# Performance work log

Measured on AMD Instinct MI355X. Metric: run time of the kernel, lower is better.

## Reference

```python
import jax, jax.numpy as jnp
import numpy as np

N, B, C, H = 1024, 4, 256, 8
D = C // H


def _make_boxes(k):
    u = jax.random.uniform(k, (N, 4), dtype=jnp.float32)
    x1 = u[:, 0] * 500.0
    y1 = u[:, 1] * 500.0
    x2 = x1 + u[:, 2] * 200.0 + 1.0
    y2 = y1 + u[:, 3] * 200.0 + 1.0
    return jnp.stack([x1, y1, x2, y2], axis=1)


def setup_inputs() -> dict:
    rng = jax.random.key(0)
    ks = jax.random.split(rng, 10)
    s = 1.0 / np.sqrt(C)
    return {
        "query": jax.random.normal(ks[0], (N, B, C), dtype=jnp.float32),
        "key": jax.random.normal(ks[1], (N, B, C), dtype=jnp.float32),
        "value": jax.random.normal(ks[2], (N, B, C), dtype=jnp.float32),
        "q_boxes": _make_boxes(ks[3]),
        "k_boxes": _make_boxes(ks[4]),
        "Wq": jax.random.normal(ks[5], (C, C), dtype=jnp.float32) * s,
        "Wk": jax.random.normal(ks[6], (C, C), dtype=jnp.float32) * s,
        "Wv": jax.random.normal(ks[7], (C, C), dtype=jnp.float32) * s,
        "pos_w": jax.random.normal(ks[8], (H, 64), dtype=jnp.float32) * 0.125,
        "pos_b": jax.random.normal(ks[9], (H,), dtype=jnp.float32) * 0.01,
    }


def _position_bias(qb, kb, pos_w, pos_b):
    # extract_position_matrix: boxes are x1y1x2y2, shapes [N,4]
    cx, cy = 0.5 * (qb[:, 0] + qb[:, 2]), 0.5 * (qb[:, 1] + qb[:, 3])
    w, h = qb[:, 2] - qb[:, 0] + 1.0, qb[:, 3] - qb[:, 1] + 1.0
    cxr, cyr = 0.5 * (kb[:, 0] + kb[:, 2]), 0.5 * (kb[:, 1] + kb[:, 3])
    wr, hr = kb[:, 2] - kb[:, 0] + 1.0, kb[:, 3] - kb[:, 1] + 1.0
    dx = jnp.log(jnp.abs((cx[:, None] - cxr[None, :]) / w[:, None]) + 1e-3)
    dy = jnp.log(jnp.abs((cy[:, None] - cyr[None, :]) / h[:, None]) + 1e-3)
    dw = jnp.log(w[:, None] / wr[None, :])
    dh = jnp.log(h[:, None] / hr[None, :])
    pm = jnp.stack([dx, dy, dw, dh], axis=2)  # [N, N, 4]
    # extract_position_embedding: feat_dim=64 -> 8 sinusoid frequencies
    dim_mat = 1000.0 ** (jnp.arange(8, dtype=jnp.float32) * (8.0 / 64.0))
    div = pm[..., None] * 100.0 / dim_mat  # [N, N, 4, 8]
    emb = jnp.concatenate([jnp.sin(div), jnp.cos(div)], axis=3)
    emb = emb.reshape(pm.shape[0], pm.shape[1], 64)  # [N, N, 64]
    # 1x1 Conv2d(64 -> H) over the [64, N, N] map == channel matmul
    pe = jnp.einsum('nmc,hc->hnm', emb, pos_w) + pos_b[:, None, None]
    return jnp.log(jax.nn.relu(pe) + 1e-6)  # [H, N, N]


def reference(query, key, value, q_boxes, k_boxes, Wq, Wk, Wv, pos_w, pos_b):
    n, b, c = query.shape
    d = c // H

    def proj(x, W):
        # nn.Linear (no bias): x @ W.T ; reshape (N,B,H,D) -> (B,H,N,D)
        return (x @ W.T).reshape(n, b, H, d).transpose(1, 2, 0, 3)

    q = proj(query, Wq)
    k = proj(key, Wk)
    v = proj(value, Wv)
    # cosine normalization of q and k
    q = q / jnp.linalg.norm(q, axis=-1, keepdims=True)
    k = k / jnp.linalg.norm(k, axis=-1, keepdims=True)
    attn_reg = jax.nn.softmax(jnp.einsum('bhnd,bhmd->bhnm', q, k), axis=-1)
    # log of relu'd conv position embedding added AFTER softmax (as in source)
    attn = attn_reg + _position_bias(q_boxes, k_boxes, pos_w, pos_b)[None]
    out = jnp.einsum('bhnm,bhmd->bhnd', attn, v)  # [B,H,N,D]
    out = out.transpose(0, 2, 1, 3).reshape(b, n, c).transpose(1, 0, 2)  # [N,B,C]
    return (out, attn)
```

## Files before the change

kernel.cpp:

```cpp
#include <hip/hip_runtime.h>
#include <hip/hip_bf16.h>
#include <math.h>

#define PN 1024
#define PB 4
#define PC 256
#define PH 8
#define PD 32

typedef __attribute__((ext_vector_type(8))) short bf16x8;
typedef __attribute__((ext_vector_type(4))) float f32x4;

__device__ __forceinline__ unsigned short f2b(float f) {
    unsigned int u = __builtin_bit_cast(unsigned int, f);
    unsigned int r = (u + 0x7fffu + ((u >> 16) & 1u)) >> 16;
    return (unsigned short)r;
}
__device__ __forceinline__ float b2f(unsigned short u) {
    return __builtin_bit_cast(float, ((unsigned int)u) << 16);
}

__global__ __launch_bounds__(256) void cvt_kernel(
    const float* __restrict__ q, const float* __restrict__ k, const float* __restrict__ v,
    const float* __restrict__ wq, const float* __restrict__ wk, const float* __restrict__ wv,
    unsigned short* __restrict__ xq, unsigned short* __restrict__ xk, unsigned short* __restrict__ xv,
    unsigned short* __restrict__ wqb, unsigned short* __restrict__ wkb, unsigned short* __restrict__ wvb)
{
    int g = blockIdx.x * 256 + threadIdx.x;
    const float* src; unsigned short* dst; int off;
    if (g < 262144)      { src = q; dst = xq; off = g; }
    else if (g < 524288) { src = k; dst = xk; off = g - 262144; }
    else if (g < 786432) { src = v; dst = xv; off = g - 524288; }
    else {
        int r = g - 786432; int t = r >> 14; off = r & 16383;
        src = (t == 0) ? wq : (t == 1) ? wk : wv;
        dst = (t == 0) ? wqb : (t == 1) ? wkb : wvb;
    }
    float4 f = ((const float4*)src)[off];
    ushort4 o; o.x = f2b(f.x); o.y = f2b(f.y); o.z = f2b(f.z); o.w = f2b(f.w);
    ((ushort4*)dst)[off] = o;
}

__global__ __launch_bounds__(256) void proj_mfma(
    const unsigned short* __restrict__ xq, const unsigned short* __restrict__ xk, const unsigned short* __restrict__ xv,
    const unsigned short* __restrict__ wq, const unsigned short* __restrict__ wk, const unsigned short* __restrict__ wv,
    unsigned short* __restrict__ qb, unsigned short* __restrict__ kb, unsigned short* __restrict__ vt)
{
    const int z = blockIdx.z;
    const unsigned short* X = (z == 0) ? xq : (z == 1) ? xk : xv;
    const unsigned short* W = (z == 0) ? wq : (z == 1) ? wk : wv;

    const int row0 = blockIdx.x * 64, col0 = blockIdx.y * 64;
    const int tid = threadIdx.x;
    const int w = tid >> 6, l = tid & 63;
    const int l15 = l & 15, lg = l >> 4;
    const int wm = w >> 1, wn = w & 1;

    f32x4 acc[2][2];
    #pragma unroll
    for (int a = 0; a < 2; a++)
        #pragma unroll
        for (int b = 0; b < 2; b++) acc[a][b] = (f32x4){0.f, 0.f, 0.f, 0.f};

    #pragma unroll
    for (int ks = 0; ks < 8; ks++) {
        int koff = ks * 32 + lg * 8;
        bf16x8 a0 = *(const bf16x8*)(X + (size_t)(row0 + wm * 32 + l15) * 256 + koff);
        bf16x8 a1 = *(const bf16x8*)(X + (size_t)(row0 + wm * 32 + 16 + l15) * 256 + koff);
        bf16x8 b0 = *(const bf16x8*)(W + (size_t)(col0 + wn * 32 + l15) * 256 + koff);
        bf16x8 b1 = *(const bf16x8*)(W + (size_t)(col0 + wn * 32 + 16 + l15) * 256 + koff);
        acc[0][0] = __builtin_amdgcn_mfma_f32_16x16x32_bf16(a0, b0, acc[0][0], 0, 0, 0);
        acc[0][1] = __builtin_amdgcn_mfma_f32_16x16x32_bf16(a0, b1, acc[0][1], 0, 0, 0);
        acc[1][0] = __builtin_amdgcn_mfma_f32_16x16x32_bf16(a1, b0, acc[1][0], 0, 0, 0);
        acc[1][1] = __builtin_amdgcn_mfma_f32_16x16x32_bf16(a1, b1, acc[1][1], 0, 0, 0);
    }

    #pragma unroll
    for (int as = 0; as < 2; as++) {
        #pragma unroll
        for (int bs = 0; bs < 2; bs++) {
            #pragma unroll
            for (int r = 0; r < 4; r++) {
                int Xrow = row0 + wm * 32 + as * 16 + lg * 4 + r;
                int c = col0 + wn * 32 + bs * 16 + l15;
                int n = Xrow >> 2, bb = Xrow & 3, hh = c >> 5, dd = c & 31;
                unsigned short val = f2b(acc[as][bs][r]);
                if (z == 0)      qb[((size_t)((bb * 8 + hh) * 1024 + n)) * 32 + dd] = val;
                else if (z == 1) kb[((size_t)((bb * 8 + hh) * 1024 + n)) * 32 + dd] = val;
                else             vt[((size_t)((bb * 8 + hh) * 32 + dd)) * 1024 + n] = val;
            }
        }
    }
}

__global__ __launch_bounds__(256) void norm_kernel(unsigned short* __restrict__ qb,
                                                   unsigned short* __restrict__ kb)
{
    int idx = blockIdx.x * 256 + threadIdx.x;
    unsigned short* p = (idx < 32768) ? qb + (size_t)idx * 32
                                      : kb + (size_t)(idx - 32768) * 32;
    const unsigned int* pu = (const unsigned int*)p;
    float g[32]; float s2 = 0.f;
    #pragma unroll
    for (int j = 0; j < 16; j++) {
        unsigned int u = pu[j];
        g[2 * j]     = b2f((unsigned short)(u & 0xffff));
        g[2 * j + 1] = b2f((unsigned short)(u >> 16));
        s2 += g[2 * j] * g[2 * j] + g[2 * j + 1] * g[2 * j + 1];
    }
    float inv = rsqrtf(s2);
    unsigned int* po = (unsigned int*)p;
    #pragma unroll
    for (int j = 0; j < 16; j++) {
        unsigned int lo = f2b(g[2 * j] * inv);
        unsigned int hi = f2b(g[2 * j + 1] * inv);
        po[j] = lo | (hi << 16);
    }
}

__global__ __launch_bounds__(256) void bias_kernel(
    const float* __restrict__ qbx, const float* __restrict__ kbx,
    const float* __restrict__ pw, const float* __restrict__ pb,
    unsigned short* __restrict__ biasb)
{
    __shared__ float4 pwS[128];
    __shared__ float pbS[8];
    int tid = threadIdx.x;
    if (tid < 128) pwS[tid] = ((const float4*)pw)[tid];
    if (tid < 8) pbS[tid] = pb[tid];
    __syncthreads();

    int idx = blockIdx.x * 256 + tid;
    int n = idx >> 10, m = idx & 1023;

    float4 qx = ((const float4*)qbx)[n];
    float4 kx = ((const float4*)kbx)[m];

    float cx = 0.5f * (qx.x + qx.z), cy = 0.5f * (qx.y + qx.w);
    float w  = qx.z - qx.x + 1.0f,   hh = qx.w - qx.y + 1.0f;
    float cxr = 0.5f * (kx.x + kx.z), cyr = 0.5f * (kx.y + kx.w);
    float wr  = kx.z - kx.x + 1.0f,   hr  = kx.w - kx.y + 1.0f;

    float pm[4];
    pm[0] = __logf(fabsf((cx - cxr) / w) + 1e-3f);
    pm[1] = __logf(fabsf((cy - cyr) / hh) + 1e-3f);
    pm[2] = __logf(w / wr);
    pm[3] = __logf(hh / hr);

    const float inv[8] = {100.f, 42.1696503f, 17.7827941f, 7.49894209f,
                          3.16227766f, 1.33352143f, 0.562341325f, 0.237137371f};

    float emb[64];
    #pragma unroll
    for (int p = 0; p < 4; p++) {
        #pragma unroll
        for (int i = 0; i < 8; i++) {
            float a = pm[p] * inv[i];
            emb[p * 16 + i]     = __sinf(a);
            emb[p * 16 + 8 + i] = __cosf(a);
        }
    }

    #pragma unroll
    for (int h = 0; h < PH; h++) {
        float acc = pbS[h];
        #pragma unroll
        for (int c4 = 0; c4 < 16; c4++) {
            float4 w4 = pwS[h * 16 + c4];
            acc += emb[c4 * 4 + 0] * w4.x + emb[c4 * 4 + 1] * w4.y
                 + emb[c4 * 4 + 2] * w4.z + emb[c4 * 4 + 3] * w4.w;
        }
        float bv = __logf(fmaxf(acc, 0.f) + 1e-6f);
        biasb[((size_t)(h * 1024 + n)) * 1024 + m] = f2b(bv);
    }
}

#define SBS 1032

__global__ __launch_bounds__(512, 4) void attn_kernel(
    const unsigned short* __restrict__ qb, const unsigned short* __restrict__ kb,
    const unsigned short* __restrict__ vt, const unsigned short* __restrict__ biasb,
    float* __restrict__ out, float* __restrict__ attn_out)
{
    __shared__ unsigned short Sb[32][SBS];
    __shared__ float part[8][16][17];

    const int bh = blockIdx.y;
    const int b = bh >> 3, h = bh & 7;
    const int n0 = blockIdx.x * 32;
    const int tid = threadIdx.x;
    const int w = tid >> 6, l = tid & 63;
    const int l15 = l & 15, lg = l >> 4;

    {
        const int wq = w >> 2, wk = w & 3;
        const int qrow = n0 + wq * 16 + l15;
        bf16x8 aq = *(const bf16x8*)(qb + ((size_t)(bh << 10) + qrow) * 32 + lg * 8);
        #pragma unroll 4
        for (int t = 0; t < 16; ++t) {
            int key = wk * 256 + t * 16 + l15;
            bf16x8 bk = *(const bf16x8*)(kb + ((size_t)(bh << 10) + key) * 32 + lg * 8);
            f32x4 acc = (f32x4){0.f, 0.f, 0.f, 0.f};
            acc = __builtin_amdgcn_mfma_f32_16x16x32_bf16(aq, bk, acc, 0, 0, 0);
            int colb = wk * 256 + t * 16 + l15;
            #pragma unroll
            for (int r = 0; r < 4; ++r)
                Sb[wq * 16 + lg * 4 + r][colb] = f2b(acc[r]);
        }
    }
    __syncthreads();

    {
        for (int rr = 0; rr < 4; ++rr) {
            int r = w * 4 + rr;
            float s[16];
            #pragma unroll
            for (int i = 0; i < 16; ++i) s[i] = b2f(Sb[r][l + 64 * i]);
            float mx = s[0];
            #pragma unroll
            for (int i = 1; i < 16; ++i) mx = fmaxf(mx, s[i]);
            #pragma unroll
            for (int off = 32; off > 0; off >>= 1) mx = fmaxf(mx, __shfl_xor(mx, off));
            float e[16], sum = 0.f;
            #pragma unroll
            for (int i = 0; i < 16; ++i) { e[i] = __expf(s[i] - mx); sum += e[i]; }
            #pragma unroll
            for (int off = 32; off > 0; off >>= 1) sum += __shfl_xor(sum, off);
            float invs = 1.f / sum;

            const unsigned short* brow = biasb + ((size_t)(h * 1024 + n0 + r)) * 1024;
            float* arow = attn_out + ((size_t)(bh * 1024 + n0 + r)) * 1024;
            #pragma unroll
            for (int i = 0; i < 16; ++i) {
                int m = l + 64 * i;
                float a = e[i] * invs + b2f(brow[m]);
                arow[m] = a;
                Sb[r][m] = f2b(a);
            }
        }
    }
    __syncthreads();

    {
        const int tile = w >> 1, kh = w & 1;
        const int qs = tile >> 1, ds = tile & 1;
        f32x4 acc = (f32x4){0.f, 0.f, 0.f, 0.f};
        const unsigned short* vrow = vt + ((size_t)(bh * 32 + ds * 16 + l15) << 10);
        const unsigned short* srow = &Sb[qs * 16 + l15][0];
        #pragma unroll 4
        for (int st = 0; st < 16; ++st) {
            int m0 = kh * 512 + st * 32 + lg * 8;
            bf16x8 ap = *(const bf16x8*)(srow + m0);
            bf16x8 bv = *(const bf16x8*)(vrow + m0);
            acc = __builtin_amdgcn_mfma_f32_16x16x32_bf16(ap, bv, acc, 0, 0, 0);
        }
        #pragma unroll
        for (int r = 0; r < 4; ++r) part[w][lg * 4 + r][l15] = acc[r];
    }
    __syncthreads();

    {
        #pragma unroll
        for (int e = 0; e < 2; ++e) {
            int idx = tid + e * 512;
            int q = idx >> 5, d = idx & 31;
            int w0 = ((q >> 4) * 2 + (d >> 4)) << 1;
            float v = part[w0][q & 15][d & 15] + part[w0 + 1][q & 15][d & 15];
            out[((size_t)(n0 + q) * PB + b) * PC + h * PD + d] = v;
        }
    }
}

extern "C" void kernel_launch(void* const* d_in, const int* in_sizes, int n_in,
                              void* d_out, int out_size, void* d_ws, size_t ws_size,
                              hipStream_t stream)
{
    const float* query   = (const float*)d_in[0];
    const float* key     = (const float*)d_in[1];
    const float* value   = (const float*)d_in[2];
    const float* q_boxes = (const float*)d_in[3];
    const float* k_boxes = (const float*)d_in[4];
    const float* Wq      = (const float*)d_in[5];
    const float* Wk      = (const float*)d_in[6];
    const float* Wv      = (const float*)d_in[7];
    const float* pos_w   = (const float*)d_in[8];
    const float* pos_b   = (const float*)d_in[9];

    unsigned short* u = (unsigned short*)d_ws;
    unsigned short* xq  = u;
    unsigned short* xk  = xq + 1048576;
    unsigned short* xv  = xk + 1048576;
    unsigned short* wqb = xv + 1048576;
    unsigned short* wkb = wqb + 65536;
    unsigned short* wvb = wkb + 65536;
    unsigned short* qbf = wvb + 65536;
    unsigned short* kbf = qbf + 1048576;
    unsigned short* vtb = kbf + 1048576;
    unsigned short* bias = vtb + 1048576;

    float* out  = (float*)d_out;
    float* attn = out + (size_t)PN * PB * PC;

    cvt_kernel<<<dim3(3264), 256, 0, stream>>>(query, key, value, Wq, Wk, Wv,
                                               xq, xk, xv, wqb, wkb, wvb);
    proj_mfma<<<dim3(64, 4, 3), 256, 0, stream>>>(xq, xk, xv, wqb, wkb, wvb,
                                                  qbf, kbf, vtb);
    norm_kernel<<<dim3(256), 256, 0, stream>>>(qbf, kbf);
    bias_kernel<<<dim3(4096), 256, 0, stream>>>(q_boxes, k_boxes, pos_w, pos_b, bias);
    attn_kernel<<<dim3(32, 32), 512, 0, stream>>>(qbf, kbf, vtb, bias, out, attn);
}
```

Measured before the change: 235.4 us.

## Fuse bf16 conversion and cosine norm into projection; halve attention query tile

Removes the separate fp32-to-bf16 conversion kernel by converting inline during the projection loads. It also moves the per-head L2 normalization of q and k into the projection epilogue using lane shuffles, which eliminates a second kernel and its global round trip. The attention kernel now processes 16 query rows per block instead of 32, doubling the grid and cutting shared memory use per block, which can raise occupancy. The cost is that fp32 inputs are read twice as wide inside the projection, and K/V loads are repeated across more blocks.

```diff
diff --git a/kernel.cpp b/kernel.cpp
--- a/kernel.cpp
+++ b/kernel.cpp
@@ -19,36 +19,25 @@
 __device__ __forceinline__ float b2f(unsigned short u) {
     return __builtin_bit_cast(float, ((unsigned int)u) << 16);
 }
-
-__global__ __launch_bounds__(256) void cvt_kernel(
-    const float* __restrict__ q, const float* __restrict__ k, const float* __restrict__ v,
+__device__ __forceinline__ bf16x8 ldf8(const float* p) {
+    float4 u0 = ((const float4*)p)[0];
+    float4 u1 = ((const float4*)p)[1];
+    bf16x8 r;
+    r[0] = (short)f2b(u0.x); r[1] = (short)f2b(u0.y);
+    r[2] = (short)f2b(u0.z); r[3] = (short)f2b(u0.w);
+    r[4] = (short)f2b(u1.x); r[5] = (short)f2b(u1.y);
+    r[6] = (short)f2b(u1.z); r[7] = (short)f2b(u1.w);
+    return r;
+}
+
+__global__ __launch_bounds__(256) void proj_mfma(
+    const float* __restrict__ xq, const float* __restrict__ xk, const float* __restrict__ xv,
     const float* __restrict__ wq, const float* __restrict__ wk, const float* __restrict__ wv,
-    unsigned short* __restrict__ xq, unsigned short* __restrict__ xk, unsigned short* __restrict__ xv,
-    unsigned short* __restrict__ wqb, unsigned short* __restrict__ wkb, unsigned short* __restrict__ wvb)
-{
-    int g = blockIdx.x * 256 + threadIdx.x;
-    const float* src; unsigned short* dst; int off;
-    if (g < 262144)      { src = q; dst = xq; off = g; }
-    else if (g < 524288) { src = k; dst = xk; off = g - 262144; }
-    else if (g < 786432) { src = v; dst = xv; off = g - 524288; }
-    else {
-        int r = g - 786432; int t = r >> 14; off = r & 16383;
-        src = (t == 0) ? wq : (t == 1) ? wk : wv;
-        dst = (t == 0) ? wqb : (t == 1) ? wkb : wvb;
-    }
-    float4 f = ((const float4*)src)[off];
-    ushort4 o; o.x = f2b(f.x); o.y = f2b(f.y); o.z = f2b(f.z); o.w = f2b(f.w);
-    ((ushort4*)dst)[off] = o;
-}
-
-__global__ __launch_bounds__(256) void proj_mfma(
-    const unsigned short* __restrict__ xq, const unsigned short* __restrict__ xk, const unsigned short* __restrict__ xv,
-    const unsigned short* __restrict__ wq, const unsigned short* __restrict__ wk, const unsigned short* __restrict__ wv,
     unsigned short* __restrict__ qb, unsigned short* __restrict__ kb, unsigned short* __restrict__ vt)
 {
     const int z = blockIdx.z;
-    const unsigned short* X = (z == 0) ? xq : (z == 1) ? xk : xv;
-    const unsigned short* W = (z == 0) ? wq : (z == 1) ? wk : wv;
+    const float* X = (z == 0) ? xq : (z == 1) ? xk : xv;
+    const float* W = (z == 0) ? wq : (z == 1) ? wk : wv;
 
     const int row0 = blockIdx.x * 64, col0 = blockIdx.y * 64;
     const int tid = threadIdx.x;
@@ -65,14 +54,31 @@
     #pragma unroll
     for (int ks = 0; ks < 8; ks++) {
         int koff = ks * 32 + lg * 8;
-        bf16x8 a0 = *(const bf16x8*)(X + (size_t)(row0 + wm * 32 + l15) * 256 + koff);
-        bf16x8 a1 = *(const bf16x8*)(X + (size_t)(row0 + wm * 32 + 16 + l15) * 256 + koff);
-        bf16x8 b0 = *(const bf16x8*)(W + (size_t)(col0 + wn * 32 + l15) * 256 + koff);
-        bf16x8 b1 = *(const bf16x8*)(W + (size_t)(col0 + wn * 32 + 16 + l15) * 256 + koff);
+        bf16x8 a0 = ldf8(X + (size_t)(row0 + wm * 32 + l15) * 256 + koff);
+        bf16x8 a1 = ldf8(X + (size_t)(row0 + wm * 32 + 16 + l15) * 256 + koff);
+        bf16x8 b0 = ldf8(W + (size_t)(col0 + wn * 32 + l15) * 256 + koff);
+        bf16x8 b1 = ldf8(W + (size_t)(col0 + wn * 32 + 16 + l15) * 256 + koff);
         acc[0][0] = __builtin_amdgcn_mfma_f32_16x16x32_bf16(a0, b0, acc[0][0], 0, 0, 0);
         acc[0][1] = __builtin_amdgcn_mfma_f32_16x16x32_bf16(a0, b1, acc[0][1], 0, 0, 0);
         acc[1][0] = __builtin_amdgcn_mfma_f32_16x16x32_bf16(a1, b0, acc[1][0], 0, 0, 0);
         acc[1][1] = __builtin_amdgcn_mfma_f32_16x16x32_bf16(a1, b1, acc[1][1], 0, 0, 0);
+    }
+
+    if (z < 2) {
+        #pragma unroll
+        for (int as = 0; as < 2; as++) {
+            #pragma unroll
+            for (int r = 0; r < 4; r++) {
+                float ss = acc[as][0][r] * acc[as][0][r] + acc[as][1][r] * acc[as][1][r];
+                ss += __shfl_xor(ss, 1);
+                ss += __shfl_xor(ss, 2);
+                ss += __shfl_xor(ss, 4);
+                ss += __shfl_xor(ss, 8);
+                float inv = rsqrtf(ss);
+                acc[as][0][r] *= inv;
+                acc[as][1][r] *= inv;
+            }
+        }
     }
 
     #pragma unroll
@@ -93,31 +99,6 @@
     }
 }
 
-__global__ __launch_bounds__(256) void norm_kernel(unsigned short* __restrict__ qb,
-                                                   unsigned short* __restrict__ kb)
-{
-    int idx = blockIdx.x * 256 + threadIdx.x;
-    unsigned short* p = (idx < 32768) ? qb + (size_t)idx * 32
-                                      : kb + (size_t)(idx - 32768) * 32;
-    const unsigned int* pu = (const unsigned int*)p;
-    float g[32]; float s2 = 0.f;
-    #pragma unroll
-    for (int j = 0; j < 16; j++) {
-        unsigned int u = pu[j];
-        g[2 * j]     = b2f((unsigned short)(u & 0xffff));
-        g[2 * j + 1] = b2f((unsigned short)(u >> 16));
-        s2 += g[2 * j] * g[2 * j] + g[2 * j + 1] * g[2 * j + 1];
-    }
-    float inv = rsqrtf(s2);
-    unsigned int* po = (unsigned int*)p;
-    #pragma unroll
-    for (int j = 0; j < 16; j++) {
-        unsigned int lo = f2b(g[2 * j] * inv);
-        unsigned int hi = f2b(g[2 * j + 1] * inv);
-        po[j] = lo | (hi << 16);
-    }
-}
-
 __global__ __launch_bounds__(256) void bias_kernel(
     const float* __restrict__ qbx, const float* __restrict__ kbx,
     const float* __restrict__ pw, const float* __restrict__ pb,
@@ -182,37 +163,36 @@
     const unsigned short* __restrict__ vt, const unsigned short* __restrict__ biasb,
     float* __restrict__ out, float* __restrict__ attn_out)
 {
-    __shared__ unsigned short Sb[32][SBS];
+    __shared__ unsigned short Sb[16][SBS];
     __shared__ float part[8][16][17];
 
     const int bh = blockIdx.y;
     const int b = bh >> 3, h = bh & 7;
-    const int n0 = blockIdx.x * 32;
+    const int n0 = blockIdx.x * 16;
     const int tid = threadIdx.x;
     const int w = tid >> 6, l = tid & 63;
     const int l15 = l & 15, lg = l >> 4;
 
     {
-        const int wq = w >> 2, wk = w & 3;
-        const int qrow = n0 + wq * 16 + l15;
+        const int qrow = n0 + l15;
         bf16x8 aq = *(const bf16x8*)(qb + ((size_t)(bh << 10) + qrow) * 32 + lg * 8);
-        #pragma unroll 4
-        for (int t = 0; t < 16; ++t) {
-            int key = wk * 256 + t * 16 + l15;
+        #pragma unroll
+        for (int t = 0; t < 8; ++t) {
+            int key = w * 128 + t * 16 + l15;
             bf16x8 bk = *(const bf16x8*)(kb + ((size_t)(bh << 10) + key) * 32 + lg * 8);
             f32x4 acc = (f32x4){0.f, 0.f, 0.f, 0.f};
             acc = __builtin_amdgcn_mfma_f32_16x16x32_bf16(aq, bk, acc, 0, 0, 0);
-            int colb = wk * 256 + t * 16 + l15;
             #pragma unroll
             for (int r = 0; r < 4; ++r)
-                Sb[wq * 16 + lg * 4 + r][colb] = f2b(acc[r]);
-        }
-    }
-    __syncthreads();
-
-    {
-        for (int rr = 0; rr < 4; ++rr) {
-            int r = w * 4 + rr;
+                Sb[lg * 4 + r][key] = f2b(acc[r]);
+        }
+    }
+    __syncthreads();
+
+    {
+        #pragma unroll
+        for (int rr = 0; rr < 2; ++rr) {
+            int r = w * 2 + rr;
             float s[16];
             #pragma unroll
             for (int i = 0; i < 16; ++i) s[i] = b2f(Sb[r][l + 64 * i]);
@@ -242,14 +222,13 @@
     __syncthreads();
 
     {
-        const int tile = w >> 1, kh = w & 1;
-        const int qs = tile >> 1, ds = tile & 1;
+        const int ds = w >> 2, kh = w & 3;
         f32x4 acc = (f32x4){0.f, 0.f, 0.f, 0.f};
         const unsigned short* vrow = vt + ((size_t)(bh * 32 + ds * 16 + l15) << 10);
-        const unsigned short* srow = &Sb[qs * 16 + l15][0];
-        #pragma unroll 4
-        for (int st = 0; st < 16; ++st) {
-            int m0 = kh * 512 + st * 32 + lg * 8;
+        const unsigned short* srow = &Sb[l15][0];
+        #pragma unroll
+        for (int st = 0; st < 8; ++st) {
+            int m0 = kh * 256 + st * 32 + lg * 8;
             bf16x8 ap = *(const bf16x8*)(srow + m0);
             bf16x8 bv = *(const bf16x8*)(vrow + m0);
             acc = __builtin_amdgcn_mfma_f32_16x16x32_bf16(ap, bv, acc, 0, 0, 0);
@@ -260,14 +239,11 @@
     __syncthreads();
 
     {
-        #pragma unroll
-        for (int e = 0; e < 2; ++e) {
-            int idx = tid + e * 512;
-            int q = idx >> 5, d = idx & 31;
-            int w0 = ((q >> 4) * 2 + (d >> 4)) << 1;
-            float v = part[w0][q & 15][d & 15] + part[w0 + 1][q & 15][d & 15];
-            out[((size_t)(n0 + q) * PB + b) * PC + h * PD + d] = v;
-        }
+        int q = tid >> 5, d = tid & 31;
+        int ds = d >> 4, d15 = d & 15;
+        float v = part[ds * 4 + 0][q][d15] + part[ds * 4 + 1][q][d15]
+                + part[ds * 4 + 2][q][d15] + part[ds * 4 + 3][q][d15];
+        out[((size_t)(n0 + q) * PB + b) * PC + h * PD + d] = v;
     }
 }
 
@@ -287,25 +263,16 @@
     const float* pos_b   = (const float*)d_in[9];
 
     unsigned short* u = (unsigned short*)d_ws;
-    unsigned short* xq  = u;
-    unsigned short* xk  = xq + 1048576;
-    unsigned short* xv  = xk + 1048576;
-    unsigned short* wqb = xv + 1048576;
-    unsigned short* wkb = wqb + 65536;
-    unsigned short* wvb = wkb + 65536;
-    unsigned short* qbf = wvb + 65536;
-    unsigned short* kbf = qbf + 1048576;
-    unsigned short* vtb = kbf + 1048576;
+    unsigned short* qbf  = u;
+    unsigned short* kbf  = qbf + 1048576;
+    unsigned short* vtb  = kbf + 1048576;
     unsigned short* bias = vtb + 1048576;
 
     float* out  = (float*)d_out;
     float* attn = out + (size_t)PN * PB * PC;
 
-    cvt_kernel<<<dim3(3264), 256, 0, stream>>>(query, key, value, Wq, Wk, Wv,
-                                               xq, xk, xv, wqb, wkb, wvb);
-    proj_mfma<<<dim3(64, 4, 3), 256, 0, stream>>>(xq, xk, xv, wqb, wkb, wvb,
+    proj_mfma<<<dim3(64, 4, 3), 256, 0, stream>>>(query, key, value, Wq, Wk, Wv,
                                                   qbf, kbf, vtb);
-    norm_kernel<<<dim3(256), 256, 0, stream>>>(qbf, kbf);
     bias_kernel<<<dim3(4096), 256, 0, stream>>>(q_boxes, k_boxes, pos_w, pos_b, bias);
-    attn_kernel<<<dim3(32, 32), 512, 0, stream>>>(qbf, kbf, vtb, bias, out, attn);
-}
+    attn_kernel<<<dim3(64, 32), 512, 0, stream>>>(qbf, kbf, vtb, bias, out, attn);
+}
```

New measurement: 233.2 us. Within noise of the previous version (-1.0%).
